# Optimization experiments

Measured on AMD Instinct MI355X. Metric: run time of the kernel, lower is better.

## Reference

```python
import jax, jax.numpy as jnp
import numpy as np

B, N, C = 4, 4096, 64
TARGET = 560.0          # target_size
MIN_BOX = 5.0           # min_box_size
IOU_THR = 0.2
CONF_THR = 0.001
BOX_CONF_THR = 0.01
MAX_WH = 4096.0         # class-offset trick for class-aware NMS (YOLO-style)


def setup_inputs() -> dict:
    key = jax.random.key(0)
    k1, k2, k3, k4 = jax.random.split(key, 4)
    # proposals as xyxy boxes inside the (560,560) image, realistic sizes
    cxcy = jax.random.uniform(k1, (B, N, 2), dtype=jnp.float32) * TARGET
    wh = jax.random.uniform(k2, (B, N, 2), dtype=jnp.float32) * 100.0 + 2.0
    boxes = jnp.concatenate([cxcy - wh / 2, cxcy + wh / 2], axis=-1)  # [B,N,4]
    box_scores = jax.random.uniform(k3, (B, N), dtype=jnp.float32)    # objectness/10
    cls_preds = jax.random.uniform(k4, (B, N, C), dtype=jnp.float32)  # classifier scores
    return {"boxes": boxes, "box_scores": box_scores, "cls_preds": cls_preds}


def _pairwise_iou(b):
    # b: [N,4] xyxy -> [N,N] IoU
    area = (b[:, 2] - b[:, 0]) * (b[:, 3] - b[:, 1])
    lt = jnp.maximum(b[:, None, :2], b[None, :, :2])
    rb = jnp.minimum(b[:, None, 2:], b[None, :, 2:])
    wh = jnp.clip(rb - lt, 0.0)
    inter = wh[..., 0] * wh[..., 1]
    return inter / (area[:, None] + area[None, :] - inter + 1e-9)


def _detect_single(boxes, box_scores, cls_preds):
    # --- filter_boxes: clip to image, drop tiny boxes and low objectness ---
    b = jnp.clip(boxes, 0.0, TARGET)                       # [N,4]
    w = b[:, 2] - b[:, 0]
    h = b[:, 3] - b[:, 1]
    # YOLO-style combined confidence: objectness * per-class score
    cls_conf = cls_preds * box_scores[:, None]             # [N,C]
    conf = jnp.max(cls_conf, axis=-1)                      # [N]
    cls = jnp.argmax(cls_conf, axis=-1)                    # [N] int
    valid = ((box_scores > BOX_CONF_THR) & (w > MIN_BOX) & (h > MIN_BOX)
             & (conf > CONF_THR))
    # --- sort by confidence, descending (invalid boxes sink to bottom) ---
    score_key = jnp.where(valid, conf, -1.0)
    order = jnp.argsort(-score_key)
    b = b[order]; conf = conf[order]; cls = cls[order]; v = valid[order]
    # --- class-aware greedy NMS via per-class coordinate offset ---
    ob = b + (cls.astype(b.dtype) * MAX_WH)[:, None]
    iou = _pairwise_iou(ob)                                # [N,N]
    n = b.shape[0]
    idx = jnp.arange(n)

    def body(suppressed, i):
        keep_i = v[i] & (~suppressed[i])
        new_sup = suppressed | (keep_i & (iou[i] > IOU_THR) & (idx > i))
        return new_sup, keep_i

    _, keeps = jax.lax.scan(body, jnp.zeros(n, dtype=bool), idx)
    keep = (keeps & v).astype(b.dtype)                     # [N]
    det = jnp.concatenate([b, conf[:, None], cls.astype(b.dtype)[:, None]], -1)
    return det * keep[:, None]                             # [N,6] padded with zeros


def reference(boxes, box_scores, cls_preds):
    # [B,N,6]: (x1,y1,x2,y2,conf,class) per kept detection, zero rows otherwise
    return jax.vmap(_detect_single)(boxes, box_scores, cls_preds)
```

## Files before the change

### kernel.cpp

```cpp
#include <hip/hip_runtime.h>
#include <stdint.h>

#pragma clang fp contract(off)

typedef unsigned long long u64;
typedef unsigned int u32;
typedef unsigned short u16;

namespace {
constexpr int BB = 4;
constexpr int NN = 4096;
constexpr int CC = 64;
constexpr int BN = BB * NN;
constexpr float TARGET = 560.0f;
constexpr float MIN_BOX = 5.0f;
constexpr float IOU_THR = 0.2f;
constexpr float CONF_THR = 0.001f;
constexpr float BOX_CONF_THR = 0.01f;
constexpr float MAX_WH = 4096.0f;
constexpr int MAXK = 2048;
}

__device__ __forceinline__ void zero_row(float* __restrict__ out, int p) {
    float2* o2 = (float2*)(out + (size_t)p * 6);
    float2 z; z.x = 0.0f; z.y = 0.0f;
    o2[0] = z; o2[1] = z; o2[2] = z;
}

__device__ __forceinline__ void emit_row(float* __restrict__ out, int p,
                                         float4 bc, float cf, float cls) {
    float2* o2 = (float2*)(out + (size_t)p * 6);
    float2 aa; aa.x = bc.x; aa.y = bc.y;
    float2 cc; cc.x = bc.z; cc.y = bc.w;
    float2 ee; ee.x = cf;   ee.y = cls;
    o2[0] = aa; o2[1] = cc; o2[2] = ee;
}

__device__ __forceinline__ bool iou_gt(float4 bi, float ai, float4 bj, float aj) {
    float ltx = fmaxf(bi.x, bj.x);
    float lty = fmaxf(bi.y, bj.y);
    float rbx = fminf(bi.z, bj.z);
    float rby = fminf(bi.w, bj.w);
    float ww = fmaxf(rbx - ltx, 0.0f);
    float hh = fmaxf(rby - lty, 0.0f);
    float inter = ww * hh;
    float iou = inter / (ai + aj - inter + 1e-9f);
    return iou > IOU_THR;
}

__global__ __launch_bounds__(256) void k1_score(const float* __restrict__ boxes,
                                                const float* __restrict__ box_scores,
                                                const float* __restrict__ cls_preds,
                                                float4* __restrict__ boxes_c,
                                                float* __restrict__ conf,
                                                int* __restrict__ clsval,
                                                u64* __restrict__ key64,
                                                int* __restrict__ rank) {
    int r = (blockIdx.x << 6) + (threadIdx.x >> 2);
    int sub = threadIdx.x & 3;
    float bs = box_scores[r];
    const float4* cp = (const float4*)(cls_preds + ((size_t)r << 6) + (sub << 4));
    float best = -1.0f;
    int bestc = sub << 4;
#pragma unroll
    for (int q = 0; q < 4; ++q) {
        float4 v = cp[q];
        float p0 = v.x * bs, p1 = v.y * bs, p2 = v.z * bs, p3 = v.w * bs;
        int cb = (sub << 4) + (q << 2);
        if (p0 > best) { best = p0; bestc = cb + 0; }
        if (p1 > best) { best = p1; bestc = cb + 1; }
        if (p2 > best) { best = p2; bestc = cb + 2; }
        if (p3 > best) { best = p3; bestc = cb + 3; }
    }
#pragma unroll
    for (int d2 = 1; d2 < 4; d2 <<= 1) {
        float ob = __shfl_xor(best, d2);
        int oc = __shfl_xor(bestc, d2);
        if (ob > best || (ob == best && oc < bestc)) { best = ob; bestc = oc; }
    }
    if (sub == 0) {
        float4 bx = ((const float4*)boxes)[r];
        float x1 = fminf(fmaxf(bx.x, 0.0f), TARGET);
        float y1 = fminf(fmaxf(bx.y, 0.0f), TARGET);
        float x2 = fminf(fmaxf(bx.z, 0.0f), TARGET);
        float y2 = fminf(fmaxf(bx.w, 0.0f), TARGET);
        float w = x2 - x1, h = y2 - y1;
        bool valid = (bs > BOX_CONF_THR) && (w > MIN_BOX) && (h > MIN_BOX) && (best > CONF_THR);
        float sk = valid ? best : -1.0f;
        unsigned fb = __float_as_uint(sk);
        unsigned mm = (fb & 0x80000000u) ? ~fb : (fb | 0x80000000u);
        int i = r & (NN - 1);
        key64[r] = ((u64)mm << 12) | (u64)(NN - 1 - i);
        float4 bc; bc.x = x1; bc.y = y1; bc.z = x2; bc.w = y2;
        boxes_c[r] = bc;
        conf[r] = best;
        clsval[r] = bestc | (valid ? 0x10000 : 0);
        rank[r] = 0;
    }
}

__global__ __launch_bounds__(256) void k2_rank(const u64* __restrict__ key64,
                                               int* __restrict__ rank) {
    __shared__ u64 sk[512];
    int bid = blockIdx.x;
    int kseg = bid & 7;
    int eseg = (bid >> 3) & 15;
    int b    = bid >> 7;
    int tid = threadIdx.x;
    const u64* kb = key64 + ((size_t)b << 12);
    for (int p = tid; p < 512; p += 256) sk[p] = kb[(kseg << 9) + p];
    __syncthreads();
    int i = (eseg << 8) + tid;
    u64 my = kb[i];
    int r = 0;
    const ulonglong2* s2 = (const ulonglong2*)sk;
#pragma unroll 16
    for (int q = 0; q < 256; ++q) {
        ulonglong2 v = s2[q];
        r += (int)(v.x > my) + (int)(v.y > my);
    }
    atomicAdd(&rank[(b << 12) + i], r);
}

__global__ __launch_bounds__(64) void k3_nms(const float4* __restrict__ boxes_c,
                                             const float* __restrict__ conf,
                                             const int* __restrict__ clsval,
                                             const int* __restrict__ rank,
                                             float* __restrict__ out) {
    __shared__ u32 bitset[128];
    __shared__ u16 pos2e[NN];
    __shared__ int lpos[MAXK];
    __shared__ float4 lbox[MAXK];
    __shared__ float larea[128];
    const int lane = threadIdx.x;
    const int b = blockIdx.x >> 6;
    const int myc = blockIdx.x & 63;
    const int base = b << 12;
    const float off = (float)myc * MAX_WH;

    bitset[2 * lane] = 0;
    bitset[2 * lane + 1] = 0;
    __syncthreads();

    const int4* cvp = (const int4*)(clsval + base);
    const int4* rkp = (const int4*)(rank + base);
#pragma unroll
    for (int q = 0; q < 16; ++q) {
        int4 cv = cvp[(q << 6) + lane];
        int4 rk = rkp[(q << 6) + lane];
        int e = (q << 8) + (lane << 2);
        if ((cv.x & 0xFF) == myc) {
            if (cv.x & 0x10000) { atomicOr(&bitset[rk.x >> 5], 1u << (rk.x & 31)); pos2e[rk.x] = (u16)(e + 0); }
            else zero_row(out, base + rk.x);
        }
        if ((cv.y & 0xFF) == myc) {
            if (cv.y & 0x10000) { atomicOr(&bitset[rk.y >> 5], 1u << (rk.y & 31)); pos2e[rk.y] = (u16)(e + 1); }
            else zero_row(out, base + rk.y);
        }
        if ((cv.z & 0xFF) == myc) {
            if (cv.z & 0x10000) { atomicOr(&bitset[rk.z >> 5], 1u << (rk.z & 31)); pos2e[rk.z] = (u16)(e + 2); }
            else zero_row(out, base + rk.z);
        }
        if ((cv.w & 0xFF) == myc) {
            if (cv.w & 0x10000) { atomicOr(&bitset[rk.w >> 5], 1u << (rk.w & 31)); pos2e[rk.w] = (u16)(e + 3); }
            else zero_row(out, base + rk.w);
        }
    }
    __syncthreads();

    u64 w = ((u64)bitset[2 * lane + 1] << 32) | (u64)bitset[2 * lane];
    int cnt = (int)__popcll(w);
    int incl = cnt;
#pragma unroll
    for (int d2 = 1; d2 < 64; d2 <<= 1) {
        int t2 = __shfl_up(incl, d2);
        if (lane >= d2) incl += t2;
    }
    int kk = __shfl(incl, 63);
    {
        int d = incl - cnt;
        u64 t = w;
        while (t) {
            int b2 = (int)__builtin_ctzll(t); t &= t - 1;
            int p = (lane << 6) + b2;
            if (d < MAXK) lpos[d] = p; else zero_row(out, base + p);
            d++;
        }
    }
    if (kk > MAXK) kk = MAXK;
    if (kk == 0) return;
    __syncthreads();

    if (kk <= 128) {
        const int j0 = lane, j1 = 64 + lane;
        bool in0 = j0 < kk, in1 = j1 < kk;
        float4 box0 = {0, 0, 0, 0}, box1 = {0, 0, 0, 0};
        float a0 = 0.0f, a1 = 0.0f;
        if (in0) {
            float4 bc = boxes_c[base + pos2e[lpos[j0]]];
            box0.x = bc.x + off; box0.y = bc.y + off; box0.z = bc.z + off; box0.w = bc.w + off;
            a0 = (box0.z - box0.x) * (box0.w - box0.y);
            lbox[j0] = box0; larea[j0] = a0;
        }
        if (in1) {
            float4 bc = boxes_c[base + pos2e[lpos[j1]]];
            box1.x = bc.x + off; box1.y = bc.y + off; box1.z = bc.z + off; box1.w = bc.w + off;
            a1 = (box1.z - box1.x) * (box1.w - box1.y);
            lbox[j1] = box1; larea[j1] = a1;
        }
        __syncthreads();
        u64 r00 = 0, r10 = 0, r11 = 0;
        if (kk <= 64) {
            for (int i = 0; i < kk; ++i) {
                float4 bi = lbox[i];
                float ai = larea[i];
                bool s0 = in0 && (j0 > i) && iou_gt(bi, ai, box0, a0);
                r00 |= ((u64)s0) << i;
            }
        } else {
            for (int i = 0; i < kk; ++i) {
                float4 bi = lbox[i];
                float ai = larea[i];
                bool s0 = in0 && (j0 > i) && iou_gt(bi, ai, box0, a0);
                bool s1 = in1 && (j1 > i) && iou_gt(bi, ai, box1, a1);
                if (i < 64) { r00 |= ((u64)s0) << i; r10 |= ((u64)s1) << i; }
                else        { r11 |= ((u64)s1) << (i - 64); }
            }
        }
        u32 sup0 = 0, sup1 = 0;
        int kc = kk < 64 ? kk : 64;
        for (int i = 0; i < kc; ++i) {
            u64 f = __ballot(sup0 != 0);
            u32 km = ((f >> i) & 1ull) ? 0u : ~0u;
            sup0 |= km & (u32)((r00 >> i) & 1ull);
            sup1 |= km & (u32)((r10 >> i) & 1ull);
        }
        for (int i = 64; i < kk; ++i) {
            u64 f = __ballot(sup1 != 0);
            u32 km = ((f >> (i - 64)) & 1ull) ? 0u : ~0u;
            sup1 |= km & (u32)((r11 >> (i - 64)) & 1ull);
        }
        if (in0) {
            int p = lpos[j0]; int e = base + pos2e[p];
            if (!sup0) emit_row(out, base + p, boxes_c[e], conf[e], (float)myc);
            else zero_row(out, base + p);
        }
        if (in1) {
            int p = lpos[j1]; int e = base + pos2e[p];
            if (!sup1) emit_row(out, base + p, boxes_c[e], conf[e], (float)myc);
            else zero_row(out, base + p);
        }
    } else {
        for (int m = lane; m < kk; m += 64) {
            float4 bc = boxes_c[base + pos2e[lpos[m]]];
            float4 ob; ob.x = bc.x + off; ob.y = bc.y + off; ob.z = bc.z + off; ob.w = bc.w + off;
            lbox[m] = ob;
        }
        __syncthreads();
        u64 supw = 0;
        for (int i = 0; i < kk; ++i) {
            u64 wd = __shfl(supw, i >> 6);
            if (((wd >> (i & 63)) & 1ull) == 0ull) {
                float4 bi = lbox[i];
                float ai = (bi.z - bi.x) * (bi.w - bi.y);
                for (int jb = (i + 1) & ~63; jb < kk; jb += 64) {
                    int j = jb + lane;
                    bool s = false;
                    if (j > i && j < kk) {
                        float4 bj = lbox[j];
                        float aj = (bj.z - bj.x) * (bj.w - bj.y);
                        s = iou_gt(bi, ai, bj, aj);
                    }
                    u64 m2 = __ballot(s);
                    if (lane == (jb >> 6)) supw |= m2;
                }
            }
        }
        for (int t2 = 0; t2 * 64 < kk; ++t2) {
            int m = t2 * 64 + lane;
            u64 wd = __shfl(supw, t2);
            if (m < kk) {
                int p = lpos[m]; int e = base + pos2e[p];
                if (((wd >> lane) & 1ull) == 0ull)
                    emit_row(out, base + p, boxes_c[e], conf[e], (float)myc);
                else zero_row(out, base + p);
            }
        }
    }
}

extern "C" void kernel_launch(void* const* d_in, const int* in_sizes, int n_in,
                              void* d_out, int out_size, void* d_ws, size_t ws_size,
                              hipStream_t stream) {
    const float* boxes      = (const float*)d_in[0];
    const float* box_scores = (const float*)d_in[1];
    const float* cls_preds  = (const float*)d_in[2];

    char* ws = (char*)d_ws;
    size_t off = 0;
    float4* boxes_c = (float4*)(ws + off); off += (size_t)BN * 16;
    u64*    key64   = (u64*)(ws + off);    off += (size_t)BN * 8;
    float*  conf    = (float*)(ws + off);  off += (size_t)BN * 4;
    int*    clsval  = (int*)(ws + off);    off += (size_t)BN * 4;
    int*    rank    = (int*)(ws + off);    off += (size_t)BN * 4;

    k1_score<<<BN / 64, 256, 0, stream>>>(boxes, box_scores, cls_preds,
                                          boxes_c, conf, clsval, key64, rank);
    k2_rank<<<BB * 128, 256, 0, stream>>>(key64, rank);
    k3_nms<<<BB * CC, 64, 0, stream>>>(boxes_c, conf, clsval, rank, (float*)d_out);
}
```

Before: 103.1 us.

## Build per-class membership bitmasks and 32-bit rank keys to shrink NMS scan

```diff
diff --git a/kernel.cpp b/kernel.cpp
--- a/kernel.cpp
+++ b/kernel.cpp
@@ -18,7 +18,7 @@
 constexpr float CONF_THR = 0.001f;
 constexpr float BOX_CONF_THR = 0.01f;
 constexpr float MAX_WH = 4096.0f;
-constexpr int MAXK = 2048;
+constexpr int MAXB = 1024;
 }
 
 __device__ __forceinline__ void zero_row(float* __restrict__ out, int p) {
@@ -34,6 +34,10 @@
     float2 cc; cc.x = bc.z; cc.y = bc.w;
     float2 ee; ee.x = cf;   ee.y = cls;
     o2[0] = aa; o2[1] = cc; o2[2] = ee;
+}
+
+__device__ __forceinline__ float conf_of(u32 mm) {
+    return __uint_as_float(mm & 0x7FFFFFFFu);
 }
 
 __device__ __forceinline__ bool iou_gt(float4 bi, float ai, float4 bj, float aj) {
@@ -52,10 +56,11 @@
                                                 const float* __restrict__ box_scores,
                                                 const float* __restrict__ cls_preds,
                                                 float4* __restrict__ boxes_c,
-                                                float* __restrict__ conf,
-                                                int* __restrict__ clsval,
-                                                u64* __restrict__ key64,
-                                                int* __restrict__ rank) {
+                                                u32* __restrict__ key32,
+                                                int* __restrict__ rank,
+                                                u64* __restrict__ clsmask,
+                                                int* __restrict__ kvb) {
+    __shared__ u32 cvs[64];
     int r = (blockIdx.x << 6) + (threadIdx.x >> 2);
     int sub = threadIdx.x & 3;
     float bs = box_scores[r];
@@ -89,81 +94,93 @@
         float sk = valid ? best : -1.0f;
         unsigned fb = __float_as_uint(sk);
         unsigned mm = (fb & 0x80000000u) ? ~fb : (fb | 0x80000000u);
-        int i = r & (NN - 1);
-        key64[r] = ((u64)mm << 12) | (u64)(NN - 1 - i);
-        float4 bc; bc.x = x1; bc.y = y1; bc.z = x2; bc.w = y2;
-        boxes_c[r] = bc;
-        conf[r] = best;
-        clsval[r] = bestc | (valid ? 0x10000 : 0);
+        key32[r] = mm;
+        float4 bc4; bc4.x = x1; bc4.y = y1; bc4.z = x2; bc4.w = y2;
+        boxes_c[r] = bc4;
         rank[r] = 0;
-    }
-}
-
-__global__ __launch_bounds__(256) void k2_rank(const u64* __restrict__ key64,
-                                               int* __restrict__ rank) {
-    __shared__ u64 sk[512];
+        cvs[threadIdx.x >> 2] = (u32)bestc | (valid ? 256u : 0u);
+    }
+    if (threadIdx.x == 0) kvb[blockIdx.x >> 6] = 0;
+    __syncthreads();
+    if (threadIdx.x < 64) {
+        u32 s = cvs[threadIdx.x];
+        int cls = (int)(s & 255u);
+        bool v = (s & 256u) != 0u;
+        u64 mym = 0;
+        for (int c = 0; c < 64; ++c) {
+            u64 m = __ballot(v && (cls == c));
+            if (threadIdx.x == c) mym = m;
+        }
+        int b = blockIdx.x >> 6, g = blockIdx.x & 63;
+        clsmask[(((size_t)(b << 6) + (size_t)threadIdx.x) << 6) + g] = mym;
+    }
+}
+
+__global__ __launch_bounds__(256) void k2_rank(const u32* __restrict__ key32,
+                                               int* __restrict__ rank,
+                                               int* __restrict__ kvb) {
     int bid = blockIdx.x;
     int kseg = bid & 7;
     int eseg = (bid >> 3) & 15;
     int b    = bid >> 7;
-    int tid = threadIdx.x;
-    const u64* kb = key64 + ((size_t)b << 12);
-    for (int p = tid; p < 512; p += 256) sk[p] = kb[(kseg << 9) + p];
-    __syncthreads();
-    int i = (eseg << 8) + tid;
-    u64 my = kb[i];
+    int lane = threadIdx.x & 63;
+    const u32* kb = key32 + ((size_t)b << 12);
+    int i = (eseg << 8) + threadIdx.x;
+    u32 my = kb[i];
+    const u32* ks = kb + (kseg << 9);
     int r = 0;
-    const ulonglong2* s2 = (const ulonglong2*)sk;
-#pragma unroll 16
-    for (int q = 0; q < 256; ++q) {
-        ulonglong2 v = s2[q];
-        r += (int)(v.x > my) + (int)(v.y > my);
+    u32 kl = ks[lane];
+    for (int c = 0; c < 8; ++c) {
+        u32 nxt = (c < 7) ? ks[((c + 1) << 6) + lane] : 0u;
+        int lim = i - ((kseg << 9) + (c << 6));
+#pragma unroll
+        for (int t = 0; t < 64; ++t) {
+            u32 bk = __shfl(kl, t);
+            r += (int)(bk > my) + (int)((bk == my) & (t < lim));
+        }
+        kl = nxt;
     }
     atomicAdd(&rank[(b << 12) + i], r);
+    if (kseg == 0) {
+        u64 bal = __ballot(my >= 0x80000000u);
+        if (lane == 0) atomicAdd(&kvb[b], (int)__popcll(bal));
+    }
 }
 
 __global__ __launch_bounds__(64) void k3_nms(const float4* __restrict__ boxes_c,
-                                             const float* __restrict__ conf,
-                                             const int* __restrict__ clsval,
+                                             const u32* __restrict__ key32,
                                              const int* __restrict__ rank,
+                                             const u64* __restrict__ clsmask,
+                                             const int* __restrict__ kvb,
                                              float* __restrict__ out) {
     __shared__ u32 bitset[128];
     __shared__ u16 pos2e[NN];
-    __shared__ int lpos[MAXK];
-    __shared__ float4 lbox[MAXK];
-    __shared__ float larea[128];
+    __shared__ u16 lpos[MAXB];
+    __shared__ float4 lbox[MAXB];
     const int lane = threadIdx.x;
     const int b = blockIdx.x >> 6;
     const int myc = blockIdx.x & 63;
     const int base = b << 12;
     const float off = (float)myc * MAX_WH;
 
+    const int kv = kvb[b];
+    {
+        int p = kv + myc + (lane << 6);
+        if (p < NN) zero_row(out, base + p);
+    }
+
     bitset[2 * lane] = 0;
     bitset[2 * lane + 1] = 0;
     __syncthreads();
 
-    const int4* cvp = (const int4*)(clsval + base);
-    const int4* rkp = (const int4*)(rank + base);
-#pragma unroll
-    for (int q = 0; q < 16; ++q) {
-        int4 cv = cvp[(q << 6) + lane];
-        int4 rk = rkp[(q << 6) + lane];
-        int e = (q << 8) + (lane << 2);
-        if ((cv.x & 0xFF) == myc) {
-            if (cv.x & 0x10000) { atomicOr(&bitset[rk.x >> 5], 1u << (rk.x & 31)); pos2e[rk.x] = (u16)(e + 0); }
-            else zero_row(out, base + rk.x);
-        }
-        if ((cv.y & 0xFF) == myc) {
-            if (cv.y & 0x10000) { atomicOr(&bitset[rk.y >> 5], 1u << (rk.y & 31)); pos2e[rk.y] = (u16)(e + 1); }
-            else zero_row(out, base + rk.y);
-        }
-        if ((cv.z & 0xFF) == myc) {
-            if (cv.z & 0x10000) { atomicOr(&bitset[rk.z >> 5], 1u << (rk.z & 31)); pos2e[rk.z] = (u16)(e + 2); }
-            else zero_row(out, base + rk.z);
-        }
-        if ((cv.w & 0xFF) == myc) {
-            if (cv.w & 0x10000) { atomicOr(&bitset[rk.w >> 5], 1u << (rk.w & 31)); pos2e[rk.w] = (u16)(e + 3); }
-            else zero_row(out, base + rk.w);
+    {
+        u64 m = clsmask[(((size_t)(b << 6) + (size_t)myc) << 6) + lane];
+        while (m) {
+            int bit = (int)__builtin_ctzll(m); m &= m - 1;
+            int e = (lane << 6) + bit;
+            int rk = rank[base + e];
+            atomicOr(&bitset[rk >> 5], 1u << (rk & 31));
+            pos2e[rk] = (u16)e;
         }
     }
     __syncthreads();
@@ -183,11 +200,11 @@
         while (t) {
             int b2 = (int)__builtin_ctzll(t); t &= t - 1;
             int p = (lane << 6) + b2;
-            if (d < MAXK) lpos[d] = p; else zero_row(out, base + p);
+            if (d < MAXB) lpos[d] = (u16)p; else zero_row(out, base + p);
             d++;
         }
     }
-    if (kk > MAXK) kk = MAXK;
+    if (kk > MAXB) kk = MAXB;
     if (kk == 0) return;
     __syncthreads();
 
@@ -197,35 +214,36 @@
         float4 box0 = {0, 0, 0, 0}, box1 = {0, 0, 0, 0};
         float a0 = 0.0f, a1 = 0.0f;
         if (in0) {
-            float4 bc = boxes_c[base + pos2e[lpos[j0]]];
-            box0.x = bc.x + off; box0.y = bc.y + off; box0.z = bc.z + off; box0.w = bc.w + off;
+            float4 bc4 = boxes_c[base + pos2e[lpos[j0]]];
+            box0.x = bc4.x + off; box0.y = bc4.y + off; box0.z = bc4.z + off; box0.w = bc4.w + off;
             a0 = (box0.z - box0.x) * (box0.w - box0.y);
-            lbox[j0] = box0; larea[j0] = a0;
         }
         if (in1) {
-            float4 bc = boxes_c[base + pos2e[lpos[j1]]];
-            box1.x = bc.x + off; box1.y = bc.y + off; box1.z = bc.z + off; box1.w = bc.w + off;
+            float4 bc4 = boxes_c[base + pos2e[lpos[j1]]];
+            box1.x = bc4.x + off; box1.y = bc4.y + off; box1.z = bc4.z + off; box1.w = bc4.w + off;
             a1 = (box1.z - box1.x) * (box1.w - box1.y);
-            lbox[j1] = box1; larea[j1] = a1;
-        }
-        __syncthreads();
+        }
         u64 r00 = 0, r10 = 0, r11 = 0;
-        if (kk <= 64) {
-            for (int i = 0; i < kk; ++i) {
-                float4 bi = lbox[i];
-                float ai = larea[i];
-                bool s0 = in0 && (j0 > i) && iou_gt(bi, ai, box0, a0);
-                r00 |= ((u64)s0) << i;
+        int k0 = kk < 64 ? kk : 64;
+        for (int i = 0; i < k0; ++i) {
+            float4 bi; float ai;
+            bi.x = __shfl(box0.x, i); bi.y = __shfl(box0.y, i);
+            bi.z = __shfl(box0.z, i); bi.w = __shfl(box0.w, i);
+            ai = __shfl(a0, i);
+            bool s0 = in0 && (j0 > i) && iou_gt(bi, ai, box0, a0);
+            r00 |= ((u64)s0) << i;
+            if (kk > 64) {
+                bool s1 = in1 && iou_gt(bi, ai, box1, a1);
+                r10 |= ((u64)s1) << i;
             }
-        } else {
-            for (int i = 0; i < kk; ++i) {
-                float4 bi = lbox[i];
-                float ai = larea[i];
-                bool s0 = in0 && (j0 > i) && iou_gt(bi, ai, box0, a0);
-                bool s1 = in1 && (j1 > i) && iou_gt(bi, ai, box1, a1);
-                if (i < 64) { r00 |= ((u64)s0) << i; r10 |= ((u64)s1) << i; }
-                else        { r11 |= ((u64)s1) << (i - 64); }
-            }
+        }
+        for (int i = 64; i < kk; ++i) {
+            float4 bi; float ai;
+            bi.x = __shfl(box1.x, i - 64); bi.y = __shfl(box1.y, i - 64);
+            bi.z = __shfl(box1.z, i - 64); bi.w = __shfl(box1.w, i - 64);
+            ai = __shfl(a1, i - 64);
+            bool s1 = in1 && (j1 > i) && iou_gt(bi, ai, box1, a1);
+            r11 |= ((u64)s1) << (i - 64);
         }
         u32 sup0 = 0, sup1 = 0;
         int kc = kk < 64 ? kk : 64;
@@ -242,18 +260,18 @@
         }
         if (in0) {
             int p = lpos[j0]; int e = base + pos2e[p];
-            if (!sup0) emit_row(out, base + p, boxes_c[e], conf[e], (float)myc);
+            if (!sup0) emit_row(out, base + p, boxes_c[e], conf_of(key32[e]), (float)myc);
             else zero_row(out, base + p);
         }
         if (in1) {
             int p = lpos[j1]; int e = base + pos2e[p];
-            if (!sup1) emit_row(out, base + p, boxes_c[e], conf[e], (float)myc);
+            if (!sup1) emit_row(out, base + p, boxes_c[e], conf_of(key32[e]), (float)myc);
             else zero_row(out, base + p);
         }
     } else {
         for (int m = lane; m < kk; m += 64) {
-            float4 bc = boxes_c[base + pos2e[lpos[m]]];
-            float4 ob; ob.x = bc.x + off; ob.y = bc.y + off; ob.z = bc.z + off; ob.w = bc.w + off;
+            float4 bc4 = boxes_c[base + pos2e[lpos[m]]];
+            float4 ob; ob.x = bc4.x + off; ob.y = bc4.y + off; ob.z = bc4.z + off; ob.w = bc4.w + off;
             lbox[m] = ob;
         }
         __syncthreads();
@@ -282,7 +300,7 @@
             if (m < kk) {
                 int p = lpos[m]; int e = base + pos2e[p];
                 if (((wd >> lane) & 1ull) == 0ull)
-                    emit_row(out, base + p, boxes_c[e], conf[e], (float)myc);
+                    emit_row(out, base + p, boxes_c[e], conf_of(key32[e]), (float)myc);
                 else zero_row(out, base + p);
             }
         }
@@ -299,13 +317,13 @@
     char* ws = (char*)d_ws;
     size_t off = 0;
     float4* boxes_c = (float4*)(ws + off); off += (size_t)BN * 16;
-    u64*    key64   = (u64*)(ws + off);    off += (size_t)BN * 8;
-    float*  conf    = (float*)(ws + off);  off += (size_t)BN * 4;
-    int*    clsval  = (int*)(ws + off);    off += (size_t)BN * 4;
+    u32*    key32   = (u32*)(ws + off);    off += (size_t)BN * 4;
     int*    rank    = (int*)(ws + off);    off += (size_t)BN * 4;
+    u64*    clsmask = (u64*)(ws + off);    off += (size_t)BB * 64 * CC * 8;
+    int*    kvb     = (int*)(ws + off);    off += (size_t)BB * 4;
 
     k1_score<<<BN / 64, 256, 0, stream>>>(boxes, box_scores, cls_preds,
-                                          boxes_c, conf, clsval, key64, rank);
-    k2_rank<<<BB * 128, 256, 0, stream>>>(key64, rank);
-    k3_nms<<<BB * CC, 64, 0, stream>>>(boxes_c, conf, clsval, rank, (float*)d_out);
-}
+                                          boxes_c, key32, rank, clsmask, kvb);
+    k2_rank<<<BB * 128, 256, 0, stream>>>(key32, rank, kvb);
+    k3_nms<<<BB * CC, 64, 0, stream>>>(boxes_c, key32, rank, clsmask, kvb, (float*)d_out);
+}
```

New measurement: 117.5 us. 1.14x slower.
